# Performance work log

Hardware: AMD Instinct MI355X
Metric: run time of the kernel (lower is better)

The kernel has to match this reference:

```python
import jax, jax.numpy as jnp
import numpy as np

CE_WEIGHT = 1.0
TRIPLET_WEIGHT = 0.1
MARGIN = 0.2


def setup_inputs() -> dict:
    key = jax.random.key(0)
    k1, k2, k3 = jax.random.split(key, 3)
    B, D, V = 4096, 512, 6000
    logits = jax.random.normal(k1, (B, V), dtype=jnp.float32)
    embeddings = jax.random.normal(k2, (B, D), dtype=jnp.float32)
    labels = jax.random.randint(k3, (B,), 0, 512, dtype=jnp.int64)
    return {"logits": logits, "embeddings": embeddings, "labels": labels}


def _pairwise_dist(emb):
    # Euclidean cdist via gram matrix; safe sqrt (zero grad where d2 == 0).
    sq = jnp.sum(emb * emb, axis=-1)  # [B]
    d2 = sq[:, None] + sq[None, :] - 2.0 * (emb @ emb.T)  # [B, B]
    d2 = jnp.maximum(d2, 0.0)
    safe = jnp.where(d2 > 0.0, d2, 1.0)
    return jnp.where(d2 > 0.0, jnp.sqrt(safe), 0.0)


def _losses(logits, embeddings, labels):
    B = logits.shape[0]
    # Cross entropy (mean reduction, matching nn.CrossEntropyLoss).
    logp = jax.nn.log_softmax(logits, axis=-1)
    ce_loss = -jnp.mean(jnp.take_along_axis(logp, labels[:, None], axis=1)[:, 0])

    # Batch-hard triplet loss, fully vectorized (one masked amax/amin per row).
    dist = _pairwise_dist(embeddings)  # [B, B]
    same = labels[:, None] == labels[None, :]  # [B, B]
    eye = jnp.eye(B, dtype=bool)
    pos_mask = same & ~eye
    neg_mask = ~same
    neg_inf = jnp.float32(-np.inf)
    pos_inf = jnp.float32(np.inf)
    hardest_pos = jnp.max(jnp.where(pos_mask, dist, neg_inf), axis=1)  # [B]
    hardest_neg = jnp.min(jnp.where(neg_mask, dist, pos_inf), axis=1)  # [B]
    valid = jnp.any(pos_mask, axis=1) & jnp.any(neg_mask, axis=1)  # [B]
    per_row = jax.nn.relu(hardest_pos - hardest_neg + MARGIN)
    per_row = jnp.where(valid, per_row, 0.0)
    n_valid = jnp.sum(valid.astype(jnp.float32))
    triplet_loss = jnp.where(n_valid > 0, jnp.sum(per_row) / jnp.maximum(n_valid, 1.0), 0.0)

    total_loss = CE_WEIGHT * ce_loss + TRIPLET_WEIGHT * triplet_loss
    return total_loss, ce_loss, triplet_loss


def reference(logits, embeddings, labels):
    return _losses(logits, embeddings, labels)
```

## Files before the change

kernel.cpp:

```cpp
#include <hip/hip_runtime.h>
#include <hip/hip_bf16.h>
#include <math.h>

#define BN   4096
#define DN   512
#define VN   6000
#define NCLS 512

typedef __attribute__((ext_vector_type(8)))  short short8;
typedef __attribute__((ext_vector_type(16))) float f32x16;

__device__ __forceinline__ unsigned short f2bf(float x) {
  unsigned int u = __float_as_uint(x);
  u = (u + 0x7FFFu + ((u >> 16) & 1u)) >> 16;
  return (unsigned short)u;
}

__device__ __forceinline__ void gld_lds16(const unsigned short* g, unsigned short* l) {
  __builtin_amdgcn_global_load_lds(
      (const __attribute__((address_space(1))) void*)g,
      (__attribute__((address_space(3))) void*)l, 16, 0, 0);
}

__launch_bounds__(256)
__global__ void prep_kernel(const float* __restrict__ emb, const int* __restrict__ labels,
                            unsigned short* __restrict__ embh, float* __restrict__ sqn,
                            int* __restrict__ cnt, int* __restrict__ posb,
                            int* __restrict__ negb) {
  const int row  = blockIdx.x * 4 + (threadIdx.x >> 6);
  const int lane = threadIdx.x & 63;
  const float4* rp = (const float4*)(emb + (size_t)row * DN);
  float4 a = rp[lane];
  float4 b = rp[lane + 64];
  float ss = a.x * a.x + a.y * a.y + a.z * a.z + a.w * a.w
           + b.x * b.x + b.y * b.y + b.z * b.z + b.w * b.w;
  ushort4 ha, hb;
  ha.x = f2bf(a.x); ha.y = f2bf(a.y); ha.z = f2bf(a.z); ha.w = f2bf(a.w);
  hb.x = f2bf(b.x); hb.y = f2bf(b.y); hb.z = f2bf(b.z); hb.w = f2bf(b.w);
  ushort4* wp = (ushort4*)(embh + (size_t)row * DN);
  wp[lane] = ha;
  wp[lane + 64] = hb;
#pragma unroll
  for (int off = 1; off < 64; off <<= 1) ss += __shfl_xor(ss, off);
  if (lane == 0) {
    sqn[row] = ss;
    posb[row] = 0;
    negb[row] = 0x7F800000;
    atomicAdd(cnt + labels[row], 1);
  }
}

__device__ __forceinline__ void triplet_job(int t, unsigned short* sA, unsigned short* sB,
                                            const unsigned short* __restrict__ embh,
                                            const float* __restrict__ sqn,
                                            const int* __restrict__ labels,
                                            int* __restrict__ posb,
                                            int* __restrict__ negb, int lane) {
  const int m = lane & 31;
  const int half = lane >> 5;

  int J = (int)((sqrtf(8.f * (float)t + 1.f) - 1.f) * 0.5f);
  while ((J + 1) * (J + 2) / 2 <= t) ++J;
  while (J * (J + 1) / 2 > t) --J;
  const int I = t - J * (J + 1) / 2;
  const int i0 = I * 64, j0 = J * 64;

  const int lrow = lane >> 3;
  const int lchk = (lane & 7) ^ lrow;
  const unsigned short* gA = embh + (size_t)(i0 + lrow) * DN + lchk * 8;
  const unsigned short* gB = embh + (size_t)(j0 + lrow) * DN + lchk * 8;

  f32x16 acc[2][2] = {};

  for (int ks = 0; ks < 8; ++ks) {
    const int kk = ks * 64;
    asm volatile("s_waitcnt lgkmcnt(0)" ::: "memory");
#pragma unroll
    for (int s = 0; s < 8; ++s)
      gld_lds16(gA + kk + (size_t)s * 8 * DN, &sA[s * 8 * 64]);
#pragma unroll
    for (int s = 0; s < 8; ++s)
      gld_lds16(gB + kk + (size_t)s * 8 * DN, &sB[s * 8 * 64]);
    asm volatile("s_waitcnt vmcnt(0)" ::: "memory");
#pragma unroll
    for (int q = 0; q < 4; ++q) {
      const int c = q * 2 + half;
      const int sw = ((c ^ (m & 7)) * 8);
      short8 a0 = *(const short8*)&sA[m * 64 + sw];
      short8 a1 = *(const short8*)&sA[(32 + m) * 64 + sw];
      short8 b0 = *(const short8*)&sB[m * 64 + sw];
      short8 b1 = *(const short8*)&sB[(32 + m) * 64 + sw];
      acc[0][0] = __builtin_amdgcn_mfma_f32_32x32x16_bf16(a0, b0, acc[0][0], 0, 0, 0);
      acc[0][1] = __builtin_amdgcn_mfma_f32_32x32x16_bf16(a0, b1, acc[0][1], 0, 0, 0);
      acc[1][0] = __builtin_amdgcn_mfma_f32_32x32x16_bf16(a1, b0, acc[1][0], 0, 0, 0);
      acc[1][1] = __builtin_amdgcn_mfma_f32_32x32x16_bf16(a1, b1, acc[1][1], 0, 0, 0);
    }
  }

  const int gjc0 = j0 + m, gjc1 = j0 + 32 + m;
  const int clab0 = labels[gjc0], clab1 = labels[gjc1];
  const float csq0 = sqn[gjc0], csq1 = sqn[gjc1];
  float pc0 = 0.f, pc1 = 0.f, nc0 = INFINITY, nc1 = INFINITY;

#pragma unroll
  for (int rb = 0; rb < 2; ++rb) {
#pragma unroll
    for (int r = 0; r < 16; ++r) {
      const int gi = i0 + rb * 32 + (r & 3) + 8 * (r >> 2) + 4 * half;
      const int rl = labels[gi];
      const float rq = sqn[gi];
      const float d0 = fmaf(-2.f, acc[rb][0][r], rq + csq0);
      const float d1 = fmaf(-2.f, acc[rb][1][r], rq + csq1);
      float prow = 0.f, nrow = INFINITY;
      const bool same0 = (rl == clab0), self0 = (gi == gjc0);
      const bool same1 = (rl == clab1), self1 = (gi == gjc1);
      if (same0) {
        if (!self0) { pc0 = fmaxf(pc0, d0); prow = fmaxf(prow, d0); }
      } else { nc0 = fminf(nc0, d0); nrow = fminf(nrow, d0); }
      if (same1) {
        if (!self1) { pc1 = fmaxf(pc1, d1); prow = fmaxf(prow, d1); }
      } else { nc1 = fminf(nc1, d1); nrow = fminf(nrow, d1); }
#pragma unroll
      for (int off = 1; off < 32; off <<= 1) {
        prow = fmaxf(prow, __shfl_xor(prow, off));
        nrow = fminf(nrow, __shfl_xor(nrow, off));
      }
      if (m == 0) {
        atomicMax(posb + gi, __float_as_int(prow));
        atomicMin(negb + gi, __float_as_int(nrow));
      }
    }
  }
  pc0 = fmaxf(pc0, __shfl_xor(pc0, 32)); nc0 = fminf(nc0, __shfl_xor(nc0, 32));
  pc1 = fmaxf(pc1, __shfl_xor(pc1, 32)); nc1 = fminf(nc1, __shfl_xor(nc1, 32));
  if (half == 0) {
    atomicMax(posb + gjc0, __float_as_int(pc0));
    atomicMin(negb + gjc0, __float_as_int(nc0));
    atomicMax(posb + gjc1, __float_as_int(pc1));
    atomicMin(negb + gjc1, __float_as_int(nc1));
  }
}

__launch_bounds__(64, 3)
__global__ void fused_kernel(const float* __restrict__ logits,
                             const int* __restrict__ labels,
                             float* __restrict__ ce_part,
                             const unsigned short* __restrict__ embh,
                             const float* __restrict__ sqn,
                             int* __restrict__ posb, int* __restrict__ negb) {
  __shared__ unsigned short smem[8192];
  const int b = blockIdx.x;
  const int lane = threadIdx.x;

  int trip_job, ce_row;
  if (b < 32) {
    trip_job = 2048 + b; ce_row = -1;
  } else {
    const int g = (b - 32) / 3, r = (b - 32) % 3;
    if (r == 0) { trip_job = g; ce_row = -1; }
    else        { trip_job = -1; ce_row = g * 2 + (r - 1); }
  }

  if (trip_job >= 0) {
    triplet_job(trip_job, smem, smem + 4096, embh, sqn, labels, posb, negb, lane);
    return;
  }

  const float* rp = logits + (size_t)ce_row * VN;
  const float xlab = rp[labels[ce_row]];
  const float4* q = (const float4*)rp;
  float4 v[24];
#pragma unroll
  for (int u = 0; u < 23; ++u) v[u] = q[lane + u * 64];
  if (lane < 28) v[23] = q[lane + 23 * 64];
  float s = 0.f;
#pragma unroll
  for (int u = 0; u < 23; ++u)
    s += __expf(v[u].x) + __expf(v[u].y) + __expf(v[u].z) + __expf(v[u].w);
  if (lane < 28)
    s += __expf(v[23].x) + __expf(v[23].y) + __expf(v[23].z) + __expf(v[23].w);
#pragma unroll
  for (int off = 1; off < 64; off <<= 1) s += __shfl_xor(s, off);
  if (lane == 0) ce_part[ce_row] = logf(s) - xlab;
}

__launch_bounds__(1024)
__global__ void finalize_kernel(const int* __restrict__ posb, const int* __restrict__ negb,
                                const int* __restrict__ labels, const int* __restrict__ cnt,
                                const float* __restrict__ ce_part, float* __restrict__ out) {
  const int tid = threadIdx.x;
  float cesum = 0.f, sum = 0.f, nv = 0.f;
#pragma unroll
  for (int u = 0; u < 4; ++u) {
    const int i = tid + u * 1024;
    cesum += ce_part[i];
    int c = cnt[labels[i]];
    float p = sqrtf(fmaxf(__int_as_float(posb[i]), 0.f));
    float n = sqrtf(fmaxf(__int_as_float(negb[i]), 0.f));
    float t = fmaxf(p - n + 0.2f, 0.f);
    if (c >= 2 && c < BN) { sum += t; nv += 1.f; }
  }
#pragma unroll
  for (int off = 1; off < 64; off <<= 1) {
    cesum += __shfl_xor(cesum, off);
    sum   += __shfl_xor(sum, off);
    nv    += __shfl_xor(nv, off);
  }
  __shared__ float s0[16], s1[16], s2[16];
  if ((tid & 63) == 0) { s0[tid >> 6] = cesum; s1[tid >> 6] = sum; s2[tid >> 6] = nv; }
  __syncthreads();
  if (tid == 0) {
    cesum = 0.f; sum = 0.f; nv = 0.f;
#pragma unroll
    for (int wv = 0; wv < 16; ++wv) { cesum += s0[wv]; sum += s1[wv]; nv += s2[wv]; }
    float trip = (nv > 0.f) ? sum / nv : 0.f;
    float ce = cesum * (1.f / BN);
    out[0] = ce + 0.1f * trip;
    out[1] = ce;
    out[2] = trip;
  }
}

extern "C" void kernel_launch(void* const* d_in, const int* in_sizes, int n_in,
                              void* d_out, int out_size, void* d_ws, size_t ws_size,
                              hipStream_t stream) {
  const float* logits = (const float*)d_in[0];
  const float* emb    = (const float*)d_in[1];
  const int*   labels = (const int*)d_in[2];
  float* out = (float*)d_out;

  char* ws = (char*)d_ws;
  unsigned short* embh = (unsigned short*)ws;
  float* sqn    = (float*)(ws + (size_t)BN * DN * 2);
  int*   posb   = (int*)((char*)sqn  + (size_t)BN * 4);
  int*   negb   = (int*)((char*)posb + (size_t)BN * 4);
  int*   cnt    = (int*)((char*)negb + (size_t)BN * 4);
  float* ce_part = (float*)((char*)cnt + (size_t)NCLS * 4);

  hipMemsetAsync(cnt, 0, (size_t)NCLS * 4, stream);
  hipLaunchKernelGGL(prep_kernel, dim3(BN / 4), dim3(256), 0, stream,
                     emb, labels, embh, sqn, cnt, posb, negb);
  hipLaunchKernelGGL(fused_kernel, dim3(32 + 2048 * 3), dim3(64), 0, stream,
                     logits, labels, ce_part, embh, sqn, posb, negb);
  hipLaunchKernelGGL(finalize_kernel, dim3(1), dim3(1024), 0, stream,
                     posb, negb, labels, cnt, ce_part, out);
}
```

Baseline: 191.3 us.

## Load MFMA operands directly from global memory and split CE row loads

The triplet Gram tile no longer stages bf16 embedding chunks through LDS with global_load_lds and waitcnt barriers. Each lane instead reads its short8 MFMA operands straight from global memory, relying on L2/cache reuse, which removes the 16KB shared allocation and the serialised load-wait-compute steps. The CE path loads its row in two batches separated by sched_barrier to lower register pressure. The cost is uncoalesced 16-byte strided global reads per MFMA step and heavier reliance on cache hits.

After: 219.5 us. 1.15x slower.

```diff
diff --git a/kernel.cpp b/kernel.cpp
--- a/kernel.cpp
+++ b/kernel.cpp
@@ -14,12 +14,6 @@
   unsigned int u = __float_as_uint(x);
   u = (u + 0x7FFFu + ((u >> 16) & 1u)) >> 16;
   return (unsigned short)u;
-}
-
-__device__ __forceinline__ void gld_lds16(const unsigned short* g, unsigned short* l) {
-  __builtin_amdgcn_global_load_lds(
-      (const __attribute__((address_space(1))) void*)g,
-      (__attribute__((address_space(3))) void*)l, 16, 0, 0);
 }
 
 __launch_bounds__(256)
@@ -50,7 +44,7 @@
   }
 }
 
-__device__ __forceinline__ void triplet_job(int t, unsigned short* sA, unsigned short* sB,
+__device__ __forceinline__ void triplet_job(int t,
                                             const unsigned short* __restrict__ embh,
                                             const float* __restrict__ sqn,
                                             const int* __restrict__ labels,
@@ -65,36 +59,23 @@
   const int I = t - J * (J + 1) / 2;
   const int i0 = I * 64, j0 = J * 64;
 
-  const int lrow = lane >> 3;
-  const int lchk = (lane & 7) ^ lrow;
-  const unsigned short* gA = embh + (size_t)(i0 + lrow) * DN + lchk * 8;
-  const unsigned short* gB = embh + (size_t)(j0 + lrow) * DN + lchk * 8;
+  const unsigned short* pa0 = embh + (size_t)(i0 + m) * DN + half * 8;
+  const unsigned short* pa1 = embh + (size_t)(i0 + 32 + m) * DN + half * 8;
+  const unsigned short* pb0 = embh + (size_t)(j0 + m) * DN + half * 8;
+  const unsigned short* pb1 = embh + (size_t)(j0 + 32 + m) * DN + half * 8;
 
   f32x16 acc[2][2] = {};
 
-  for (int ks = 0; ks < 8; ++ks) {
-    const int kk = ks * 64;
-    asm volatile("s_waitcnt lgkmcnt(0)" ::: "memory");
-#pragma unroll
-    for (int s = 0; s < 8; ++s)
-      gld_lds16(gA + kk + (size_t)s * 8 * DN, &sA[s * 8 * 64]);
-#pragma unroll
-    for (int s = 0; s < 8; ++s)
-      gld_lds16(gB + kk + (size_t)s * 8 * DN, &sB[s * 8 * 64]);
-    asm volatile("s_waitcnt vmcnt(0)" ::: "memory");
-#pragma unroll
-    for (int q = 0; q < 4; ++q) {
-      const int c = q * 2 + half;
-      const int sw = ((c ^ (m & 7)) * 8);
-      short8 a0 = *(const short8*)&sA[m * 64 + sw];
-      short8 a1 = *(const short8*)&sA[(32 + m) * 64 + sw];
-      short8 b0 = *(const short8*)&sB[m * 64 + sw];
-      short8 b1 = *(const short8*)&sB[(32 + m) * 64 + sw];
-      acc[0][0] = __builtin_amdgcn_mfma_f32_32x32x16_bf16(a0, b0, acc[0][0], 0, 0, 0);
-      acc[0][1] = __builtin_amdgcn_mfma_f32_32x32x16_bf16(a0, b1, acc[0][1], 0, 0, 0);
-      acc[1][0] = __builtin_amdgcn_mfma_f32_32x32x16_bf16(a1, b0, acc[1][0], 0, 0, 0);
-      acc[1][1] = __builtin_amdgcn_mfma_f32_32x32x16_bf16(a1, b1, acc[1][1], 0, 0, 0);
-    }
+#pragma unroll 4
+  for (int kk = 0; kk < DN; kk += 16) {
+    short8 a0 = *(const short8*)(pa0 + kk);
+    short8 a1 = *(const short8*)(pa1 + kk);
+    short8 b0 = *(const short8*)(pb0 + kk);
+    short8 b1 = *(const short8*)(pb1 + kk);
+    acc[0][0] = __builtin_amdgcn_mfma_f32_32x32x16_bf16(a0, b0, acc[0][0], 0, 0, 0);
+    acc[0][1] = __builtin_amdgcn_mfma_f32_32x32x16_bf16(a0, b1, acc[0][1], 0, 0, 0);
+    acc[1][0] = __builtin_amdgcn_mfma_f32_32x32x16_bf16(a1, b0, acc[1][0], 0, 0, 0);
+    acc[1][1] = __builtin_amdgcn_mfma_f32_32x32x16_bf16(a1, b1, acc[1][1], 0, 0, 0);
   }
 
   const int gjc0 = j0 + m, gjc1 = j0 + 32 + m;
@@ -148,7 +129,6 @@
                              const unsigned short* __restrict__ embh,
                              const float* __restrict__ sqn,
                              int* __restrict__ posb, int* __restrict__ negb) {
-  __shared__ unsigned short smem[8192];
   const int b = blockIdx.x;
   const int lane = threadIdx.x;
 
@@ -162,23 +142,35 @@
   }
 
   if (trip_job >= 0) {
-    triplet_job(trip_job, smem, smem + 4096, embh, sqn, labels, posb, negb, lane);
+    triplet_job(trip_job, embh, sqn, labels, posb, negb, lane);
     return;
   }
 
   const float* rp = logits + (size_t)ce_row * VN;
   const float xlab = rp[labels[ce_row]];
   const float4* q = (const float4*)rp;
-  float4 v[24];
-#pragma unroll
-  for (int u = 0; u < 23; ++u) v[u] = q[lane + u * 64];
-  if (lane < 28) v[23] = q[lane + 23 * 64];
   float s = 0.f;
-#pragma unroll
-  for (int u = 0; u < 23; ++u)
-    s += __expf(v[u].x) + __expf(v[u].y) + __expf(v[u].z) + __expf(v[u].w);
-  if (lane < 28)
-    s += __expf(v[23].x) + __expf(v[23].y) + __expf(v[23].z) + __expf(v[23].w);
+  {
+    float4 v[16];
+#pragma unroll
+    for (int u = 0; u < 16; ++u) v[u] = q[lane + u * 64];
+    __builtin_amdgcn_sched_barrier(0);
+#pragma unroll
+    for (int u = 0; u < 16; ++u)
+      s += __expf(v[u].x) + __expf(v[u].y) + __expf(v[u].z) + __expf(v[u].w);
+  }
+  {
+    float4 w[8];
+#pragma unroll
+    for (int u = 0; u < 7; ++u) w[u] = q[lane + (16 + u) * 64];
+    if (lane < 28) w[7] = q[lane + 23 * 64];
+    __builtin_amdgcn_sched_barrier(0);
+#pragma unroll
+    for (int u = 0; u < 7; ++u)
+      s += __expf(w[u].x) + __expf(w[u].y) + __expf(w[u].z) + __expf(w[u].w);
+    if (lane < 28)
+      s += __expf(w[7].x) + __expf(w[7].y) + __expf(w[7].z) + __expf(w[7].w);
+  }
 #pragma unroll
   for (int off = 1; off < 64; off <<= 1) s += __shfl_xor(s, off);
   if (lane == 0) ce_part[ce_row] = logf(s) - xlab;
```
